# Kernel tuning notes

Measured on AMD Instinct MI355X. Metric: run time of the kernel, lower is better.

The kernel has to match this reference:

```python
import jax, jax.numpy as jnp
import numpy as np

EPS = 1e-5

def group_norm(x, groups, w, b):
    # x: (B, C, ...) -> normalize over each group of channels + spatial dims
    B, C = x.shape[0], x.shape[1]
    xr = x.reshape(B, groups, -1)
    mu = xr.mean(-1, keepdims=True)
    var = xr.var(-1, keepdims=True)
    xn = ((xr - mu) * jax.lax.rsqrt(var + EPS)).reshape(x.shape)
    wshape = (1, C) + (1,) * (x.ndim - 2)
    return xn * w.reshape(wshape) + b.reshape(wshape)

def dwconv1d(x, w):
    # x: (B, Cg, L), w: (Cg, 1, k) depthwise, 'same' padding (odd k)
    k = w.shape[-1]
    return jax.lax.conv_general_dilated(
        x, w, window_strides=(1,), padding=[(k // 2, k // 2)],
        dimension_numbers=('NCH', 'OIH', 'NCH'),
        feature_group_count=x.shape[1])

def setup_inputs() -> dict:
    key = jax.random.key(0)
    ks = jax.random.split(key, 16)
    B, C, H, W = 32, 256, 56, 56
    Cg = C // 4
    inp = {'x': jax.random.normal(ks[0], (B, C, H, W), jnp.float32)}
    for i, k in enumerate((3, 5, 7, 9)):
        inp[f'dwh{i}'] = jax.random.normal(ks[1 + i], (Cg, 1, k), jnp.float32) * 0.2
        inp[f'dww{i}'] = jax.random.normal(ks[5 + i], (Cg, 1, k), jnp.float32) * 0.2
    inp['gnh_w'] = jnp.ones((C,), jnp.float32)
    inp['gnh_b'] = jnp.zeros((C,), jnp.float32)
    inp['gnw_w'] = jnp.ones((C,), jnp.float32)
    inp['gnw_b'] = jnp.zeros((C,), jnp.float32)
    inp['gn1_w'] = jnp.ones((C,), jnp.float32)
    inp['gn1_b'] = jnp.zeros((C,), jnp.float32)
    inp['wq'] = jax.random.normal(ks[13], (C,), jnp.float32)
    inp['wk'] = jax.random.normal(ks[14], (C,), jnp.float32)
    inp['wv'] = jax.random.normal(ks[15], (C,), jnp.float32)
    return inp

def reference(x, dwh0, dwh1, dwh2, dwh3, dww0, dww1, dww2, dww3,
              gnh_w, gnh_b, gnw_w, gnw_b, gn1_w, gn1_b, wq, wk, wv):
    B, C, H, W = x.shape
    n, Cg, p, gn_groups = 4, C // 4, 7, 4
    dwh = (dwh0, dwh1, dwh2, dwh3)
    dww = (dww0, dww1, dww2, dww3)

    # ---- SMSA: pooled multi-kernel depthwise 1D convs ----
    x_h = x.mean(axis=3)  # (B, C, H)
    x_w = x.mean(axis=2)  # (B, C, W)
    h_cat = jnp.concatenate(
        [dwconv1d(x_h[:, i * Cg:(i + 1) * Cg], dwh[i]) for i in range(n)], axis=1)
    w_cat = jnp.concatenate(
        [dwconv1d(x_w[:, i * Cg:(i + 1) * Cg], dww[i]) for i in range(n)], axis=1)
    Ah = jax.nn.sigmoid(group_norm(h_cat, gn_groups, gnh_w, gnh_b))  # (B,C,H)
    Aw = jax.nn.sigmoid(group_norm(w_cat, gn_groups, gnw_w, gnw_b))  # (B,C,W)
    x_s = x * (Ah[..., :, None] * Aw[..., None, :])  # (B,C,H,W)

    # ---- PCSA: adaptive pool to (p,p) then channel self-attention ----
    # H % p == 0 and W % p == 0, so adaptive avg pool == block mean
    xp = x_s.reshape(B, C, p, H // p, p, W // p).mean(axis=(3, 5))  # (B,C,p,p)
    xp = group_norm(xp, 1, gn1_w, gn1_b)
    N = p * p
    xf = xp.reshape(B, C, N)
    q = xf * wq[None, :, None]  # 1x1 depthwise conv == per-channel scale
    k = xf * wk[None, :, None]
    v = xf * wv[None, :, None]
    attn = jnp.einsum('bcn,bdn->bcd', q, k) / np.sqrt(float(N))
    attn = jax.nn.softmax(attn, axis=-1)
    o = jnp.einsum('bcd,bdn->bcn', attn, v)  # (B,C,N)
    Mc = jax.nn.sigmoid(o.mean(axis=-1))  # (B,C) adaptive avg pool to 1
    return x_s * Mc[:, :, None, None]
```

## Files before the change

### kernel.cpp

```cpp
#include <hip/hip_runtime.h>
#include <math.h>

#define B_  32
#define C_  256
#define H_  56
#define W_  56
#define CG_ 64
#define NG_ 4
#define P_  7
#define N_  49
#define XPP_ 52
#define PLP_ 57
#define PLANE_ (H_*W_)
#define EPS_ 1e-5f

typedef float f4v __attribute__((ext_vector_type(4)));
typedef short s4v __attribute__((ext_vector_type(4)));
typedef short s8v __attribute__((ext_vector_type(8)));
typedef unsigned int uint32;

__device__ __forceinline__ float sig_(float v) { return 1.0f / (1.0f + expf(-v)); }

__device__ __forceinline__ short f2bf_(float f) {
  uint32 u = __builtin_bit_cast(uint32, f);
  u = (u + 0x7FFFu + ((u >> 16) & 1u)) >> 16;
  return (short)u;
}
__device__ __forceinline__ float bf2f_(short s) {
  uint32 u = ((uint32)(unsigned short)s) << 16;
  return __builtin_bit_cast(float, u);
}

__global__ __launch_bounds__(256) void k1_means_bf(const float* __restrict__ x,
                                                   float* __restrict__ xh,
                                                   float* __restrict__ xw,
                                                   short* __restrict__ xbf) {
  __shared__ float pl[H_ * PLP_];
  const int bc = blockIdx.x, t = threadIdx.x;
  const f4v* src = (const f4v*)(x + (size_t)bc * PLANE_);
  s4v* bdst = (s4v*)(xbf + (size_t)bc * PLANE_);
  for (int i = t; i < PLANE_ / 4; i += 256) {
    const f4v v = src[i];
    const int h = i / 14, c4 = i % 14;
    const int base = h * PLP_ + 4 * c4;
    pl[base]     = v.x; pl[base + 1] = v.y;
    pl[base + 2] = v.z; pl[base + 3] = v.w;
    s4v b;
    b.x = f2bf_(v.x); b.y = f2bf_(v.y); b.z = f2bf_(v.z); b.w = f2bf_(v.w);
    bdst[i] = b;
  }
  __syncthreads();
  if (t < H_) {
    float s = 0.f;
    #pragma unroll
    for (int w = 0; w < W_; ++w) s += pl[t * PLP_ + w];
    xh[(size_t)bc * H_ + t] = s * (1.0f / W_);
  } else if (t >= 64 && t < 64 + W_) {
    const int w = t - 64;
    float s = 0.f;
    #pragma unroll
    for (int h = 0; h < H_; ++h) s += pl[h * PLP_ + w];
    xw[(size_t)bc * W_ + w] = s * (1.0f / H_);
  }
}

__global__ __launch_bounds__(256) void k2_convgn(
    const float* __restrict__ inh, const float* __restrict__ inw,
    float* __restrict__ Ah, float* __restrict__ Aw,
    const float* __restrict__ h0, const float* __restrict__ h1,
    const float* __restrict__ h2, const float* __restrict__ h3,
    const float* __restrict__ w0, const float* __restrict__ w1,
    const float* __restrict__ w2, const float* __restrict__ w3,
    const float* __restrict__ gnh_w, const float* __restrict__ gnh_b,
    const float* __restrict__ gnw_w, const float* __restrict__ gnw_b) {
  __shared__ float sin_[CG_ * H_];
  __shared__ float sconv[CG_ * H_];
  __shared__ float redS[4], redQ[4];
  __shared__ float sMu, sRs;
  const int g = blockIdx.x, b = blockIdx.y, zz = blockIdx.z, t = threadIdx.x;
  const float* in = zz ? inw : inh;
  float* outb = zz ? Aw : Ah;
  const float* wt = zz ? ((g == 0) ? w0 : (g == 1) ? w1 : (g == 2) ? w2 : w3)
                       : ((g == 0) ? h0 : (g == 1) ? h1 : (g == 2) ? h2 : h3);
  const float* gw = zz ? gnw_w : gnh_w;
  const float* gb = zz ? gnw_b : gnh_b;
  const size_t base = ((size_t)b * C_ + (size_t)g * CG_) * H_;
  const int k = 3 + 2 * g, pad = k / 2;
  for (int i = t; i < CG_ * H_; i += 256) sin_[i] = in[base + i];
  __syncthreads();
  float lsum = 0.f, lsq = 0.f;
  for (int i = t; i < CG_ * H_; i += 256) {
    const int cc = i / H_, l = i % H_;
    float s = 0.f;
    for (int j = 0; j < k; ++j) {
      const int ll = l + j - pad;
      if (ll >= 0 && ll < H_) s += sin_[cc * H_ + ll] * wt[cc * k + j];
    }
    sconv[i] = s;
    lsum += s; lsq += s * s;
  }
  #pragma unroll
  for (int m = 32; m >= 1; m >>= 1) { lsum += __shfl_xor(lsum, m); lsq += __shfl_xor(lsq, m); }
  if ((t & 63) == 0) { redS[t >> 6] = lsum; redQ[t >> 6] = lsq; }
  __syncthreads();
  if (t == 0) {
    const float S = redS[0] + redS[1] + redS[2] + redS[3];
    const float Q = redQ[0] + redQ[1] + redQ[2] + redQ[3];
    const float mu = S / (float)(CG_ * H_);
    sMu = mu; sRs = rsqrtf(Q / (float)(CG_ * H_) - mu * mu + EPS_);
  }
  __syncthreads();
  const float mu = sMu, rs = sRs;
  for (int i = t; i < CG_ * H_; i += 256) {
    const int c = g * CG_ + i / H_;
    outb[base + i] = sig_((sconv[i] - mu) * rs * gw[c] + gb[c]);
  }
}

__global__ __launch_bounds__(448) void k3_pool_bf(const short* __restrict__ xbf,
    const float* __restrict__ Ah, const float* __restrict__ Aw,
    float* __restrict__ xp) {
  __shared__ float ah[H_];
  __shared__ __align__(16) float aw[W_];
  __shared__ float part[H_ * P_];
  const int bc = blockIdx.x, t = threadIdx.x;
  if (t < H_) ah[t] = Ah[(size_t)bc * H_ + t];
  else if (t >= 64 && t < 64 + W_) aw[t - 64] = Aw[(size_t)bc * W_ + (t - 64)];
  __syncthreads();
  const s8v* xx = (const s8v*)(xbf + (size_t)bc * PLANE_);
  if (t < H_ * P_) {
    const int h = t / P_, pw = t % P_;
    const s8v b = xx[t];
    const f4v awa = ((const f4v*)aw)[2 * pw];
    const f4v awb = ((const f4v*)aw)[2 * pw + 1];
    float s = bf2f_(b[0]) * awa.x + bf2f_(b[1]) * awa.y
            + bf2f_(b[2]) * awa.z + bf2f_(b[3]) * awa.w
            + bf2f_(b[4]) * awb.x + bf2f_(b[5]) * awb.y
            + bf2f_(b[6]) * awb.z + bf2f_(b[7]) * awb.w;
    part[t] = s * ah[h];
  }
  __syncthreads();
  if (t < N_) {
    const int ph = t / P_, pw = t % P_;
    float s = 0.f;
    #pragma unroll
    for (int r = 0; r < 8; ++r) s += part[(8 * ph + r) * P_ + pw];
    xp[(size_t)bc * XPP_ + t] = s * (1.0f / 64.0f);
  } else if (t < XPP_) {
    xp[(size_t)bc * XPP_ + t] = 0.f;
  }
}

__global__ __launch_bounds__(256) void k4_attn(const float* __restrict__ xp,
    const float* __restrict__ gw, const float* __restrict__ gb,
    const float* __restrict__ wq, const float* __restrict__ wk, const float* __restrict__ wv,
    float* __restrict__ Mc) {
  __shared__ __align__(16) float xn[C_ * XPP_];
  __shared__ float vbar[C_];
  __shared__ float swk[C_];
  __shared__ float redS[4], redQ[4];
  __shared__ float sMu, sRs;
  const int chunk = blockIdx.x, b = blockIdx.y, t = threadIdx.x;
  const f4v* src4 = (const f4v*)(xp + (size_t)b * C_ * XPP_);
  f4v* xn4 = (f4v*)xn;

  float lsum = 0.f, lsq = 0.f;
  #pragma unroll
  for (int j = 0; j < 13; ++j) {
    const int i = t + 256 * j;
    const f4v v = src4[i];
    xn4[i] = v;
    lsum += v.x + v.y + v.z + v.w;
    lsq  += v.x * v.x + v.y * v.y + v.z * v.z + v.w * v.w;
  }
  swk[t] = wk[t];
  #pragma unroll
  for (int m = 32; m >= 1; m >>= 1) { lsum += __shfl_xor(lsum, m); lsq += __shfl_xor(lsq, m); }
  if ((t & 63) == 0) { redS[t >> 6] = lsum; redQ[t >> 6] = lsq; }
  __syncthreads();
  if (t == 0) {
    const float S = redS[0] + redS[1] + redS[2] + redS[3];
    const float Q = redQ[0] + redQ[1] + redQ[2] + redQ[3];
    const float mu = S / (float)(C_ * N_);
    sMu = mu; sRs = rsqrtf(Q / (float)(C_ * N_) - mu * mu + EPS_);
  }
  __syncthreads();
  const float mu = sMu, rs = sRs;
  #pragma unroll
  for (int j = 0; j < 13; ++j) {
    const int i = t + 256 * j;
    const int c = i / 13, kk = i - c * 13;
    f4v v = xn4[i];
    v.x = (v.x - mu) * rs * gw[c] + gb[c];
    v.y = (v.y - mu) * rs * gw[c] + gb[c];
    v.z = (v.z - mu) * rs * gw[c] + gb[c];
    v.w = (v.w - mu) * rs * gw[c] + gb[c];
    if (kk == 12) { v.y = 0.f; v.z = 0.f; v.w = 0.f; }
    xn4[i] = v;
  }
  __syncthreads();
  {
    const f4v* row = (const f4v*)&xn[t * XPP_];
    f4v a = row[0];
    #pragma unroll
    for (int j = 1; j < 13; ++j) a += row[j];
    vbar[t] = wv[t] * (a.x + a.y + a.z + a.w) * (1.0f / N_);
  }
  __syncthreads();

  const int rg = t >> 4, q16 = t & 15;
  const int c0 = chunk * 32 + rg * 2;
  f4v qa[13], qb[13];
  {
    const f4v* r0 = (const f4v*)&xn[c0 * XPP_];
    const f4v* r1 = (const f4v*)&xn[(c0 + 1) * XPP_];
    #pragma unroll
    for (int j = 0; j < 13; ++j) { qa[j] = r0[j]; qb[j] = r1[j]; }
  }
  const float qs0 = wq[c0] * (1.0f / 7.0f);
  const float qs1 = wq[c0 + 1] * (1.0f / 7.0f);

  float s0[16], s1[16], vb[16];
  #pragma unroll
  for (int dd = 0; dd < 16; ++dd) {
    const int d = q16 + 16 * dd;
    const f4v* kb = (const f4v*)&xn[d * XPP_];
    f4v a0 = {0.f, 0.f, 0.f, 0.f}, a1 = {0.f, 0.f, 0.f, 0.f};
    #pragma unroll
    for (int j = 0; j < 13; ++j) {
      const f4v kv = kb[j];
      a0 += qa[j] * kv;
      a1 += qb[j] * kv;
    }
    const float wkd = swk[d];
    s0[dd] = (a0.x + a0.y + a0.z + a0.w) * qs0 * wkd;
    s1[dd] = (a1.x + a1.y + a1.z + a1.w) * qs1 * wkd;
    vb[dd] = vbar[d];
  }
  float m0 = -INFINITY, m1 = -INFINITY;
  #pragma unroll
  for (int dd = 0; dd < 16; ++dd) { m0 = fmaxf(m0, s0[dd]); m1 = fmaxf(m1, s1[dd]); }
  #pragma unroll
  for (int msk = 1; msk < 16; msk <<= 1) {
    m0 = fmaxf(m0, __shfl_xor(m0, msk, 16));
    m1 = fmaxf(m1, __shfl_xor(m1, msk, 16));
  }
  float e0 = 0.f, a0 = 0.f, e1 = 0.f, a1 = 0.f;
  #pragma unroll
  for (int dd = 0; dd < 16; ++dd) {
    const float x0 = expf(s0[dd] - m0);
    const float x1 = expf(s1[dd] - m1);
    e0 += x0; a0 += x0 * vb[dd];
    e1 += x1; a1 += x1 * vb[dd];
  }
  #pragma unroll
  for (int msk = 1; msk < 16; msk <<= 1) {
    e0 += __shfl_xor(e0, msk, 16); a0 += __shfl_xor(a0, msk, 16);
    e1 += __shfl_xor(e1, msk, 16); a1 += __shfl_xor(a1, msk, 16);
  }
  if (q16 == 0) {
    Mc[(size_t)b * C_ + c0]     = sig_(a0 / e0);
    Mc[(size_t)b * C_ + c0 + 1] = sig_(a1 / e1);
  }
}

__global__ __launch_bounds__(448) void k5_out_bf(const short* __restrict__ xbf,
    const float* __restrict__ Ah, const float* __restrict__ Aw,
    const float* __restrict__ Mc, float* __restrict__ out) {
  __shared__ float ah[H_];
  __shared__ __align__(16) float aw[W_];
  __shared__ float smc;
  const int bc = blockIdx.x, t = threadIdx.x;
  if (t < H_) ah[t] = Ah[(size_t)bc * H_ + t];
  else if (t >= 64 && t < 64 + W_) aw[t - 64] = Aw[(size_t)bc * W_ + (t - 64)];
  else if (t == 128) smc = Mc[bc];
  __syncthreads();
  const float mc = smc;
  const s8v* xx = (const s8v*)(xbf + (size_t)bc * PLANE_);
  f4v* oo = (f4v*)(out + (size_t)bc * PLANE_);
  if (t < H_ * P_) {
    const int h = t / P_, pw = t % P_;
    const s8v b = xx[t];
    const float a = ah[h] * mc;
    const f4v awa = ((const f4v*)aw)[2 * pw];
    const f4v awb = ((const f4v*)aw)[2 * pw + 1];
    f4v o1, o2;
    o1.x = bf2f_(b[0]) * a * awa.x; o1.y = bf2f_(b[1]) * a * awa.y;
    o1.z = bf2f_(b[2]) * a * awa.z; o1.w = bf2f_(b[3]) * a * awa.w;
    o2.x = bf2f_(b[4]) * a * awb.x; o2.y = bf2f_(b[5]) * a * awb.y;
    o2.z = bf2f_(b[6]) * a * awb.z; o2.w = bf2f_(b[7]) * a * awb.w;
    oo[2 * t]     = o1;
    oo[2 * t + 1] = o2;
  }
}

extern "C" void kernel_launch(void* const* d_in, const int* in_sizes, int n_in,
                              void* d_out, int out_size, void* d_ws, size_t ws_size,
                              hipStream_t stream) {
  const float* x     = (const float*)d_in[0];
  const float* dwh0  = (const float*)d_in[1];
  const float* dww0  = (const float*)d_in[2];
  const float* dwh1  = (const float*)d_in[3];
  const float* dww1  = (const float*)d_in[4];
  const float* dwh2  = (const float*)d_in[5];
  const float* dww2  = (const float*)d_in[6];
  const float* dwh3  = (const float*)d_in[7];
  const float* dww3  = (const float*)d_in[8];
  const float* gnh_w = (const float*)d_in[9];
  const float* gnh_b = (const float*)d_in[10];
  const float* gnw_w = (const float*)d_in[11];
  const float* gnw_b = (const float*)d_in[12];
  const float* gn1_w = (const float*)d_in[13];
  const float* gn1_b = (const float*)d_in[14];
  const float* wq    = (const float*)d_in[15];
  const float* wk    = (const float*)d_in[16];
  const float* wv    = (const float*)d_in[17];
  float* out = (float*)d_out;

  float* ws   = (float*)d_ws;
  float* bufh = ws;
  float* bufw = bufh + (size_t)B_ * C_ * H_;
  float* Ah   = bufw + (size_t)B_ * C_ * W_;
  float* Aw   = Ah   + (size_t)B_ * C_ * H_;
  float* xp   = Aw   + (size_t)B_ * C_ * W_;
  float* Mc   = xp   + (size_t)B_ * C_ * XPP_;
  short* xbf  = (short*)(Mc + (size_t)B_ * C_);

  const int nbc = B_ * C_;
  k1_means_bf<<<nbc, 256, 0, stream>>>(x, bufh, bufw, xbf);
  k2_convgn<<<dim3(NG_, B_, 2), 256, 0, stream>>>(bufh, bufw, Ah, Aw,
      dwh0, dwh1, dwh2, dwh3, dww0, dww1, dww2, dww3,
      gnh_w, gnh_b, gnw_w, gnw_b);
  k3_pool_bf<<<nbc, 448, 0, stream>>>(xbf, Ah, Aw, xp);
  k4_attn<<<dim3(8, B_), 256, 0, stream>>>(xp, gn1_w, gn1_b, wq, wk, wv, Mc);
  k5_out_bf<<<nbc, 448, 0, stream>>>(xbf, Ah, Aw, Mc, out);
}
```

Before: 101.4 us.

## Process four channel planes per block in pool and output kernels, drop shared memory

The pooling and output kernels now handle four (batch, channel) planes per block instead of one, with a quarter as many blocks. Both read Ah, Aw and Mc directly from global memory instead of staging them in shared memory, so the __syncthreads barriers go away. The pooling kernel remaps threads so each wave covers one pooled row, and it reduces the eight-row partial sums with cross-lane shuffles instead of a shared-memory pass. This trims per-block launch, barrier and shared-memory overhead, at the cost of redundant global loads of the Aw/Ah vectors that must be served from cache.

```diff
diff --git a/kernel.cpp b/kernel.cpp
--- a/kernel.cpp
+++ b/kernel.cpp
@@ -12,6 +12,7 @@
 #define XPP_ 52
 #define PLP_ 57
 #define PLANE_ (H_*W_)
+#define NBC_ (B_*C_)
 #define EPS_ 1e-5f
 
 typedef float f4v __attribute__((ext_vector_type(4)));
@@ -117,37 +118,38 @@
   }
 }
 
-__global__ __launch_bounds__(448) void k3_pool_bf(const short* __restrict__ xbf,
+__global__ __launch_bounds__(448) void k3_pool_bf4(const short* __restrict__ xbf,
     const float* __restrict__ Ah, const float* __restrict__ Aw,
     float* __restrict__ xp) {
-  __shared__ float ah[H_];
-  __shared__ __align__(16) float aw[W_];
-  __shared__ float part[H_ * P_];
-  const int bc = blockIdx.x, t = threadIdx.x;
-  if (t < H_) ah[t] = Ah[(size_t)bc * H_ + t];
-  else if (t >= 64 && t < 64 + W_) aw[t - 64] = Aw[(size_t)bc * W_ + (t - 64)];
-  __syncthreads();
-  const s8v* xx = (const s8v*)(xbf + (size_t)bc * PLANE_);
-  if (t < H_ * P_) {
-    const int h = t / P_, pw = t % P_;
-    const s8v b = xx[t];
-    const f4v awa = ((const f4v*)aw)[2 * pw];
-    const f4v awb = ((const f4v*)aw)[2 * pw + 1];
-    float s = bf2f_(b[0]) * awa.x + bf2f_(b[1]) * awa.y
-            + bf2f_(b[2]) * awa.z + bf2f_(b[3]) * awa.w
-            + bf2f_(b[4]) * awb.x + bf2f_(b[5]) * awb.y
-            + bf2f_(b[6]) * awb.z + bf2f_(b[7]) * awb.w;
-    part[t] = s * ah[h];
-  }
-  __syncthreads();
-  if (t < N_) {
-    const int ph = t / P_, pw = t % P_;
+  const int t = threadIdx.x;
+  const int wv = t >> 6;
+  const int ln = t & 63;
+  const int r  = ln >> 3;
+  const int pw = ln & 7;
+  const int h  = 8 * wv + r;
+  const bool act = (pw < 7);
+  #pragma unroll
+  for (int c = 0; c < 4; ++c) {
+    const int bc = blockIdx.x * 4 + c;
     float s = 0.f;
-    #pragma unroll
-    for (int r = 0; r < 8; ++r) s += part[(8 * ph + r) * P_ + pw];
-    xp[(size_t)bc * XPP_ + t] = s * (1.0f / 64.0f);
-  } else if (t < XPP_) {
-    xp[(size_t)bc * XPP_ + t] = 0.f;
+    if (act) {
+      const s8v b = ((const s8v*)(xbf + (size_t)bc * PLANE_))[h * 7 + pw];
+      const f4v* aw4 = (const f4v*)(Aw + (size_t)bc * W_);
+      const f4v awa = aw4[2 * pw];
+      const f4v awb = aw4[2 * pw + 1];
+      const float ahh = Ah[(size_t)bc * H_ + h];
+      s = (bf2f_(b[0]) * awa.x + bf2f_(b[1]) * awa.y
+         + bf2f_(b[2]) * awa.z + bf2f_(b[3]) * awa.w
+         + bf2f_(b[4]) * awb.x + bf2f_(b[5]) * awb.y
+         + bf2f_(b[6]) * awb.z + bf2f_(b[7]) * awb.w) * ahh;
+    }
+    s += __shfl_xor(s, 8);
+    s += __shfl_xor(s, 16);
+    s += __shfl_xor(s, 32);
+    if (act && r == 0)
+      xp[(size_t)bc * XPP_ + wv * 7 + pw] = s * (1.0f / 64.0f);
+    if (wv == 6 && ln >= 56 && ln < 59)
+      xp[(size_t)bc * XPP_ + 49 + (ln - 56)] = 0.f;
   }
 }
 
@@ -264,31 +266,26 @@
   }
 }
 
-__global__ __launch_bounds__(448) void k5_out_bf(const short* __restrict__ xbf,
+__global__ __launch_bounds__(448) void k5_out_bf4(const short* __restrict__ xbf,
     const float* __restrict__ Ah, const float* __restrict__ Aw,
     const float* __restrict__ Mc, float* __restrict__ out) {
-  __shared__ float ah[H_];
-  __shared__ __align__(16) float aw[W_];
-  __shared__ float smc;
-  const int bc = blockIdx.x, t = threadIdx.x;
-  if (t < H_) ah[t] = Ah[(size_t)bc * H_ + t];
-  else if (t >= 64 && t < 64 + W_) aw[t - 64] = Aw[(size_t)bc * W_ + (t - 64)];
-  else if (t == 128) smc = Mc[bc];
-  __syncthreads();
-  const float mc = smc;
-  const s8v* xx = (const s8v*)(xbf + (size_t)bc * PLANE_);
-  f4v* oo = (f4v*)(out + (size_t)bc * PLANE_);
-  if (t < H_ * P_) {
-    const int h = t / P_, pw = t % P_;
-    const s8v b = xx[t];
-    const float a = ah[h] * mc;
-    const f4v awa = ((const f4v*)aw)[2 * pw];
-    const f4v awb = ((const f4v*)aw)[2 * pw + 1];
+  const int t = threadIdx.x;
+  if (t >= H_ * P_) return;
+  const int h = t / P_, pw = t % P_;
+  #pragma unroll
+  for (int c = 0; c < 4; ++c) {
+    const int bc = blockIdx.x * 4 + c;
+    const s8v b = ((const s8v*)(xbf + (size_t)bc * PLANE_))[t];
+    const f4v* aw4 = (const f4v*)(Aw + (size_t)bc * W_);
+    const f4v awa = aw4[2 * pw];
+    const f4v awb = aw4[2 * pw + 1];
+    const float a = Ah[(size_t)bc * H_ + h] * Mc[bc];
     f4v o1, o2;
     o1.x = bf2f_(b[0]) * a * awa.x; o1.y = bf2f_(b[1]) * a * awa.y;
     o1.z = bf2f_(b[2]) * a * awa.z; o1.w = bf2f_(b[3]) * a * awa.w;
     o2.x = bf2f_(b[4]) * a * awb.x; o2.y = bf2f_(b[5]) * a * awb.y;
     o2.z = bf2f_(b[6]) * a * awb.z; o2.w = bf2f_(b[7]) * a * awb.w;
+    f4v* oo = (f4v*)(out + (size_t)bc * PLANE_);
     oo[2 * t]     = o1;
     oo[2 * t + 1] = o2;
   }
@@ -326,12 +323,11 @@
   float* Mc   = xp   + (size_t)B_ * C_ * XPP_;
   short* xbf  = (short*)(Mc + (size_t)B_ * C_);
 
-  const int nbc = B_ * C_;
-  k1_means_bf<<<nbc, 256, 0, stream>>>(x, bufh, bufw, xbf);
+  k1_means_bf<<<NBC_, 256, 0, stream>>>(x, bufh, bufw, xbf);
   k2_convgn<<<dim3(NG_, B_, 2), 256, 0, stream>>>(bufh, bufw, Ah, Aw,
       dwh0, dwh1, dwh2, dwh3, dww0, dww1, dww2, dww3,
       gnh_w, gnh_b, gnw_w, gnw_b);
-  k3_pool_bf<<<nbc, 448, 0, stream>>>(xbf, Ah, Aw, xp);
+  k3_pool_bf4<<<NBC_ / 4, 448, 0, stream>>>(xbf, Ah, Aw, xp);
   k4_attn<<<dim3(8, B_), 256, 0, stream>>>(xp, gn1_w, gn1_b, wq, wk, wv, Mc);
-  k5_out_bf<<<nbc, 448, 0, stream>>>(xbf, Ah, Aw, Mc, out);
-}
+  k5_out_bf4<<<NBC_ / 4, 448, 0, stream>>>(xbf, Ah, Aw, Mc, out);
+}
```

Result: no change. 99.61 us (-1.7%).
